# Kernel tuning notes

Hardware: AMD Instinct MI355X
Metric: run time of the kernel (lower is better)

The kernel has to match this reference:

```python
import jax, jax.numpy as jnp
import numpy as np

DIM = 1024      # input_size (C)
E = 8           # num_experts
TOPK = 2        # use_experts
MLP = 4 * DIM   # int(dim * mlp_ratio)
B, N = 4, 1024


def _gelu(v):
    # torch nn.GELU default = exact erf gelu
    return jax.nn.gelu(v, approximate=False)


def setup_inputs() -> dict:
    key = jax.random.key(0)
    ks = jax.random.split(key, 20)
    s = 0.02
    f32 = jnp.float32
    return {
        "x": jax.random.normal(ks[0], (B, N, DIM), f32),
        "prompt": jax.random.normal(ks[1], (B, N, DIM), f32),
        "t": jax.random.uniform(ks[2], (B, N, 1), f32) * 1000.0,
        # gating time_embedding MLP
        "te_w1": jax.random.normal(ks[3], (1, DIM), f32) * s,
        "te_b1": jnp.zeros((DIM,), f32),
        "te_w2": jax.random.normal(ks[4], (DIM, DIM), f32) * s,
        "te_b2": jnp.zeros((DIM,), f32),
        "gate_w": jax.random.normal(ks[5], (3 * DIM, E), f32) * s,
        # stacked per-expert params [E, ...]
        "ex_tw1": jax.random.normal(ks[6], (E, 1, DIM), f32) * s,
        "ex_tb1": jnp.zeros((E, DIM), f32),
        "ex_tw2": jax.random.normal(ks[7], (E, DIM, DIM), f32) * s,
        "ex_tb2": jnp.zeros((E, DIM), f32),
        "ex_mw1": jax.random.normal(ks[8], (E, 2 * DIM, MLP), f32) * s,
        "ex_mb1": jnp.zeros((E, MLP), f32),
        "ex_mw2": jax.random.normal(ks[9], (E, MLP, DIM), f32) * s,
        "ex_mb2": jnp.zeros((E, DIM), f32),
    }


def _forward(x, prompt, t, te_w1, te_b1, te_w2, te_b2, gate_w,
             ex_tw1, ex_tb1, ex_tw2, ex_tb2, ex_mw1, ex_mb1, ex_mw2, ex_mb2):
    Bb, Nn, C = x.shape
    xf = x.reshape(-1, C)            # [T, C]
    pf = prompt.reshape(-1, C)
    tf = t.reshape(-1, 1)            # [T, 1]
    T = xf.shape[0]

    # noisy_gate (eval: no noise)
    t_emb = _gelu(tf @ te_w1 + te_b1) @ te_w2 + te_b2          # [T, C]
    x_cat = jnp.concatenate([xf, pf, t_emb], axis=-1)          # [T, 3C]
    logits = x_cat @ gate_w                                    # [T, E]
    top_l, top_i = jax.lax.top_k(logits, TOPK)
    gates = jnp.zeros_like(logits).at[
        jnp.arange(T)[:, None], top_i
    ].set(jax.nn.softmax(top_l, axis=1))                       # [T, E]

    # per-expert diffusion MLP, dense over experts (gate==0 contributes 0,
    # identical math to dispatch/split/index_add combine)
    te = _gelu(jnp.einsum('to,eod->etd', tf, ex_tw1) + ex_tb1[:, None, :])
    te = jnp.einsum('etd,edf->etf', te, ex_tw2) + ex_tb2[:, None, :]   # [E,T,C]
    xc = jnp.concatenate([jnp.broadcast_to(xf, (E, T, C)), te], axis=-1)  # [E,T,2C]
    h = _gelu(jnp.einsum('etc,ech->eth', xc, ex_mw1) + ex_mb1[:, None, :])
    out_e = jnp.einsum('eth,ehd->etd', h, ex_mw2) + ex_mb2[:, None, :]    # [E,T,C]

    out_f = jnp.einsum('te,etd->td', gates, out_e)             # combine
    output = out_f.reshape(Bb, Nn, C)

    load = gates.sum(0)                                        # [E]
    eps = 1e-10
    bal = jnp.var(load, ddof=1) / (jnp.mean(load) ** 2 + eps)
    moe_loss = bal + bal  # weight_balance + load_balance (same argument)
    return output, moe_loss


def reference(x, prompt, t, te_w1, te_b1, te_w2, te_b2, gate_w,
              ex_tw1, ex_tb1, ex_tw2, ex_tb2, ex_mw1, ex_mb1, ex_mw2, ex_mb2):
    return _forward(x, prompt, t, te_w1, te_b1, te_w2, te_b2, gate_w,
                    ex_tw1, ex_tb1, ex_tw2, ex_tb2, ex_mw1, ex_mb1, ex_mw2, ex_mb2)
```

## Files before the change

### kernel.cpp

```cpp
#include <hip/hip_runtime.h>
#include <cmath>

#define TTOK 4096
#define CDIM 1024
#define NE 8
#define MLPD 4096
#define PCAP (2*TTOK + NE*128)

typedef __attribute__((ext_vector_type(8))) short short8;
typedef __attribute__((ext_vector_type(8))) unsigned short us8;
typedef __attribute__((ext_vector_type(4))) float float4v;

__device__ __forceinline__ float bf2f(unsigned short h){
  return __uint_as_float(((unsigned int)h) << 16);
}
__device__ __forceinline__ unsigned short f2bf(float f){
  unsigned int u = __float_as_uint(f);
  u += 0x7FFFu + ((u >> 16) & 1u);
  return (unsigned short)(u >> 16);
}
__device__ __forceinline__ float gelu_exact(float x){
  return 0.5f * x * (1.0f + erff(x * 0.70710678118654752f));
}
__device__ __forceinline__ void gld16(const void* g, void* l){
  __builtin_amdgcn_global_load_lds((const __attribute__((address_space(1))) void*)g,
                                   (__attribute__((address_space(3))) void*)l, 16, 0, 0);
}
__device__ __forceinline__ int frag_off(int m, int qf){
  return (m*4 + ((qf + (m >> 1)) & 3)) << 3;
}
__device__ __forceinline__ void xcd_swz(int& bx, int& by){
  int gx = gridDim.x, gy = gridDim.y;
  int orig = blockIdx.y * gx + blockIdx.x;
  int chunk = (gx * gy) >> 3;
  int wg = (orig & 7) * chunk + (orig >> 3);
  bx = wg / gy;
  by = wg % gy;
}

__global__ __launch_bounds__(256) void k_zero(float* out, int n, int* counts, float* loadsum){
  int i = blockIdx.x*256 + threadIdx.x;
  if (i < n) out[i] = 0.f;
  if (i < NE){ counts[i] = 0; loadsum[i] = 0.f; }
}

__global__ __launch_bounds__(256) void k_m2(const float* __restrict__ te_w2,
    const float* __restrict__ te_b2, const float* __restrict__ gate_w,
    float* __restrict__ M2, float* __restrict__ c2){
  int idx = blockIdx.x*256 + threadIdx.x;
  if (idx < CDIM*NE){
    int i = idx >> 3, e = idx & 7;
    float s = 0.f;
    for (int j = 0; j < CDIM; j++)
      s += te_w2[(size_t)i*CDIM + j] * gate_w[(size_t)(2*CDIM + j)*NE + e];
    M2[idx] = s;
  } else if (idx < CDIM*NE + NE){
    int e = idx - CDIM*NE;
    float s = 0.f;
    for (int j = 0; j < CDIM; j++)
      s += te_b2[j] * gate_w[(size_t)(2*CDIM + j)*NE + e];
    c2[e] = s;
  }
}

__global__ __launch_bounds__(256) void k_cvt_w(const float* __restrict__ W,
    unsigned short* __restrict__ Wt, int K, int N){
  __shared__ unsigned short tile[64*66];
  int kb = blockIdx.x*64, nb = blockIdx.y*64, e = blockIdx.z;
  const float* Wp = W + (size_t)e*K*N + (size_t)kb*N + nb;
  unsigned short* Wo = Wt + (size_t)e*K*N + (size_t)nb*K + kb;
  int tid = threadIdx.x;
  int kr = tid >> 4, nc = (tid & 15)*4;
  #pragma unroll
  for (int i = 0; i < 64; i += 16){
    float4 v = *reinterpret_cast<const float4*>(Wp + (size_t)(kr + i)*N + nc);
    unsigned short* d = &tile[(kr + i)*66 + nc];
    d[0] = f2bf(v.x); d[1] = f2bf(v.y); d[2] = f2bf(v.z); d[3] = f2bf(v.w);
  }
  __syncthreads();
  int nr = tid >> 2, kc = (tid & 3)*16;
  #pragma unroll
  for (int h = 0; h < 2; h++){
    us8 o;
    #pragma unroll
    for (int j = 0; j < 8; j++) o[j] = tile[(kc + h*8 + j)*66 + nr];
    *reinterpret_cast<us8*>(Wo + (size_t)nr*K + kc + h*8) = o;
  }
}

__global__ __launch_bounds__(256) void k_gate(const float* __restrict__ x,
    const float* __restrict__ p, const float* __restrict__ t,
    const float* __restrict__ te_w1, const float* __restrict__ te_b1,
    const float* __restrict__ gate_w, const float* __restrict__ M2,
    const float* __restrict__ c2,
    int* __restrict__ ti, float* __restrict__ tg,
    int* __restrict__ counts, float* __restrict__ loadsum,
    unsigned short* __restrict__ xb){
  int tok = blockIdx.x, tid = threadIdx.x;
  float tv = t[tok];
  float acc[NE];
  #pragma unroll
  for (int e = 0; e < NE; e++) acc[e] = 0.f;
  for (int j = tid; j < CDIM; j += 256){
    float xv = x[(size_t)tok*CDIM + j];
    float pv = p[(size_t)tok*CDIM + j];
    if (xb) xb[(size_t)tok*CDIM + j] = f2bf(xv);
    float vv = gelu_exact(tv*te_w1[j] + te_b1[j]);
    const float* g0 = gate_w + (size_t)j*NE;
    const float* g1 = gate_w + (size_t)(CDIM + j)*NE;
    const float* m2 = M2 + (size_t)j*NE;
    #pragma unroll
    for (int e = 0; e < NE; e++) acc[e] += xv*g0[e] + pv*g1[e] + vv*m2[e];
  }
  __shared__ float red[256][NE];
  #pragma unroll
  for (int e = 0; e < NE; e++) red[tid][e] = acc[e];
  __syncthreads();
  for (int s = 128; s > 0; s >>= 1){
    if (tid < s){
      #pragma unroll
      for (int e = 0; e < NE; e++) red[tid][e] += red[tid+s][e];
    }
    __syncthreads();
  }
  if (tid == 0){
    float lg[NE];
    #pragma unroll
    for (int e = 0; e < NE; e++) lg[e] = red[0][e] + c2[e];
    int i1 = 0; float l1 = lg[0];
    #pragma unroll
    for (int e = 1; e < NE; e++) if (lg[e] > l1){ l1 = lg[e]; i1 = e; }
    int i2 = -1; float l2 = -3.4e38f;
    #pragma unroll
    for (int e = 0; e < NE; e++) if (e != i1 && lg[e] > l2){ l2 = lg[e]; i2 = e; }
    float ex  = expf(l2 - l1);
    float g1v = 1.f/(1.f + ex);
    float g2v = ex/(1.f + ex);
    ti[tok*2]   = i1; ti[tok*2+1] = i2;
    tg[tok*2]   = g1v; tg[tok*2+1] = g2v;
    atomicAdd(&counts[i1], 1);  atomicAdd(&counts[i2], 1);
    atomicAdd(&loadsum[i1], g1v); atomicAdd(&loadsum[i2], g2v);
  }
}

__global__ __launch_bounds__(256) void k_scan(const int* __restrict__ counts,
    int* __restrict__ poff, int* __restrict__ fillpos,
    int* __restrict__ tok_id, float* __restrict__ pgate, int* __restrict__ pe, int padg){
  __shared__ int so[NE+1];
  __shared__ int sc[NE];
  if (threadIdx.x == 0){
    int o = 0;
    for (int e = 0; e < NE; e++){
      so[e] = o; poff[e] = o; fillpos[e] = o;
      sc[e] = counts[e];
      o += (sc[e] + padg - 1) & ~(padg - 1);
    }
    so[NE] = o; poff[NE] = o;
  }
  __syncthreads();
  for (int e = 0; e < NE; e++){
    int s = so[e] + sc[e], en = so[e+1];
    for (int i = s + (int)threadIdx.x; i < en; i += 256){
      tok_id[i] = 0; pgate[i] = 0.f; pe[i] = e;
    }
  }
}

__global__ __launch_bounds__(256) void k_fill(const int* __restrict__ ti,
    const float* __restrict__ tg, int* __restrict__ fillpos,
    int* __restrict__ tok_id, float* __restrict__ pgate, int* __restrict__ pe,
    int* __restrict__ posmap){
  int tok = blockIdx.x*256 + threadIdx.x;
  if (tok >= TTOK) return;
  #pragma unroll
  for (int k = 0; k < 2; k++){
    int e = ti[tok*2 + k];
    int pos = atomicAdd(&fillpos[e], 1);
    tok_id[pos] = tok;
    pgate[pos]  = tg[tok*2 + k];
    pe[pos]     = e;
    posmap[tok*2 + k] = pos;
  }
}

__global__ __launch_bounds__(256) void k_vgelu(const float* __restrict__ t,
    const float* __restrict__ tw1, const float* __restrict__ tb1,
    const int* __restrict__ tok_id, const int* __restrict__ pe,
    const int* __restrict__ poff, unsigned short* __restrict__ vbuf){
  int idx = blockIdx.x*256 + threadIdx.x;
  int r = idx >> 10, k = idx & (CDIM - 1);
  if (r >= poff[NE]) return;
  int e = pe[r];
  float tv = t[tok_id[r]];
  float u = tv * tw1[(size_t)e*CDIM + k] + tb1[(size_t)e*CDIM + k];
  vbuf[(size_t)r*CDIM + k] = f2bf(gelu_exact(u));
}


__global__ __launch_bounds__(256,2) void k_mfma_te(
    const unsigned short* __restrict__ vbuf,
    const unsigned short* __restrict__ Wt1, const float* __restrict__ tb2,
    const int* __restrict__ poff, const int* __restrict__ pe,
    unsigned short* __restrict__ tebuf){
  __shared__ unsigned short As[128*32];
  __shared__ unsigned short Bs[128*32];
  int bx, by; xcd_swz(bx, by);
  int r0 = by * 128;
  if (r0 >= poff[NE]) return;
  int e = pe[r0];
  int n0 = bx * 128;
  int tid = threadIdx.x, lane = tid & 63, w = tid >> 6;
  const unsigned short* Bp = Wt1 + (size_t)e*CDIM*CDIM;
  int mb = (w&1)*64, nb = (w>>1)*64;
  float4v acc[4][4];
  #pragma unroll
  for (int i=0;i<4;i++)
    #pragma unroll
    for (int j=0;j<4;j++) acc[i][j] = (float4v){0.f,0.f,0.f,0.f};
  int rowA = w*32 + (lane>>2);
  int ck = (((lane & 3) - ((lane >> 3) & 3)) & 3) * 8;
  int r15 = lane & 15, qf = lane >> 4;
  for (int k0 = 0; k0 < CDIM; k0 += 32){
    __syncthreads();
    unsigned short* lA = As + (w*32)*32;
    unsigned short* lB = Bs + (w*32)*32;
    gld16(vbuf + (size_t)(r0+rowA)*CDIM + k0 + ck, lA);
    gld16(vbuf + (size_t)(r0+rowA+16)*CDIM + k0 + ck, lA + 16*32);
    gld16(Bp + (size_t)(n0+rowA)*CDIM + k0 + ck, lB);
    gld16(Bp + (size_t)(n0+rowA+16)*CDIM + k0 + ck, lB + 16*32);
    __syncthreads();
    short8 a[4], b[4];
    #pragma unroll
    for (int mi=0;mi<4;mi++) a[mi] = *(const short8*)(As + frag_off(mb+mi*16+r15, qf));
    #pragma unroll
    for (int ni=0;ni<4;ni++) b[ni] = *(const short8*)(Bs + frag_off(nb+ni*16+r15, qf));
    #pragma unroll
    for (int mi=0;mi<4;mi++)
      #pragma unroll
      for (int ni=0;ni<4;ni++)
        acc[mi][ni] = __builtin_amdgcn_mfma_f32_16x16x32_bf16(a[mi], b[ni], acc[mi][ni], 0, 0, 0);
  }
  int col = lane & 15, rq = (lane>>4)*4;
  const float* bias = tb2 + (size_t)e*CDIM + n0;
  #pragma unroll
  for (int mi=0;mi<4;mi++)
    #pragma unroll
    for (int ni=0;ni<4;ni++){
      int n = nb + ni*16 + col;
      #pragma unroll
      for (int rg=0;rg<4;rg++){
        int r = r0 + mb + mi*16 + rq + rg;
        tebuf[(size_t)r*CDIM + n0 + n] = f2bf(acc[mi][ni][rg] + bias[n]);
      }
    }
}

__global__ __launch_bounds__(256,2) void k_mfma_h(
    const unsigned short* __restrict__ xb, const unsigned short* __restrict__ tebuf,
    const unsigned short* __restrict__ Wt2, const float* __restrict__ mb1,
    const int* __restrict__ poff, const int* __restrict__ pe,
    const int* __restrict__ tok_id, unsigned short* __restrict__ hbuf){
  __shared__ unsigned short As[128*32];
  __shared__ unsigned short Bs[128*32];
  __shared__ int toks[128];
  int bx, by; xcd_swz(bx, by);
  int r0 = by * 128;
  if (r0 >= poff[NE]) return;
  int e = pe[r0];
  int n0 = bx * 128;
  int tid = threadIdx.x, lane = tid & 63, w = tid >> 6;
  if (tid < 128) toks[tid] = tok_id[r0 + tid];
  const unsigned short* Bp = Wt2 + (size_t)e*(2*CDIM)*MLPD;
  int mb = (w&1)*64, nb = (w>>1)*64;
  float4v acc[4][4];
  #pragma unroll
  for (int i=0;i<4;i++)
    #pragma unroll
    for (int j=0;j<4;j++) acc[i][j] = (float4v){0.f,0.f,0.f,0.f};
  int rowA = w*32 + (lane>>2);
  int ck = (((lane & 3) - ((lane >> 3) & 3)) & 3) * 8;
  int r15 = lane & 15, qf = lane >> 4;
  __syncthreads();
  for (int k0 = 0; k0 < 2*CDIM; k0 += 32){
    __syncthreads();
    unsigned short* lA = As + (w*32)*32;
    unsigned short* lB = Bs + (w*32)*32;
    if (k0 < CDIM){
      int tok0 = toks[rowA], tok1 = toks[rowA+16];
      gld16(xb + (size_t)tok0*CDIM + k0 + ck, lA);
      gld16(xb + (size_t)tok1*CDIM + k0 + ck, lA + 16*32);
    } else {
      gld16(tebuf + (size_t)(r0+rowA)*CDIM + (k0-CDIM) + ck, lA);
      gld16(tebuf + (size_t)(r0+rowA+16)*CDIM + (k0-CDIM) + ck, lA + 16*32);
    }
    gld16(Bp + (size_t)(n0+rowA)*(2*CDIM) + k0 + ck, lB);
    gld16(Bp + (size_t)(n0+rowA+16)*(2*CDIM) + k0 + ck, lB + 16*32);
    __syncthreads();
    short8 a[4], b[4];
    #pragma unroll
    for (int mi=0;mi<4;mi++) a[mi] = *(const short8*)(As + frag_off(mb+mi*16+r15, qf));
    #pragma unroll
    for (int ni=0;ni<4;ni++) b[ni] = *(const short8*)(Bs + frag_off(nb+ni*16+r15, qf));
    #pragma unroll
    for (int mi=0;mi<4;mi++)
      #pragma unroll
      for (int ni=0;ni<4;ni++)
        acc[mi][ni] = __builtin_amdgcn_mfma_f32_16x16x32_bf16(a[mi], b[ni], acc[mi][ni], 0, 0, 0);
  }
  int col = lane & 15, rq = (lane>>4)*4;
  const float* bias = mb1 + (size_t)e*MLPD + n0;
  #pragma unroll
  for (int mi=0;mi<4;mi++)
    #pragma unroll
    for (int ni=0;ni<4;ni++){
      int n = nb + ni*16 + col;
      #pragma unroll
      for (int rg=0;rg<4;rg++){
        int r = r0 + mb + mi*16 + rq + rg;
        hbuf[(size_t)r*MLPD + n0 + n] = f2bf(gelu_exact(acc[mi][ni][rg] + bias[n]));
      }
    }
}

__global__ __launch_bounds__(256,2) void k_mfma_out(
    const unsigned short* __restrict__ hbuf,
    const unsigned short* __restrict__ Wt3, const float* __restrict__ mb2,
    const int* __restrict__ poff, const int* __restrict__ pe,
    float* __restrict__ obuf){
  __shared__ unsigned short As[128*32];
  __shared__ unsigned short Bs[128*32];
  int bx, by; xcd_swz(bx, by);
  int r0 = by * 128;
  if (r0 >= poff[NE]) return;
  int e = pe[r0];
  int n0 = bx * 128;
  int tid = threadIdx.x, lane = tid & 63, w = tid >> 6;
  const unsigned short* Bp = Wt3 + (size_t)e*MLPD*CDIM;
  int mb = (w&1)*64, nb = (w>>1)*64;
  float4v acc[4][4];
  #pragma unroll
  for (int i=0;i<4;i++)
    #pragma unroll
    for (int j=0;j<4;j++) acc[i][j] = (float4v){0.f,0.f,0.f,0.f};
  int rowA = w*32 + (lane>>2);
  int ck = (((lane & 3) - ((lane >> 3) & 3)) & 3) * 8;
  int r15 = lane & 15, qf = lane >> 4;
  for (int k0 = 0; k0 < MLPD; k0 += 32){
    __syncthreads();
    unsigned short* lA = As + (w*32)*32;
    unsigned short* lB = Bs + (w*32)*32;
    gld16(hbuf + (size_t)(r0+rowA)*MLPD + k0 + ck, lA);
    gld16(hbuf + (size_t)(r0+rowA+16)*MLPD + k0 + ck, lA + 16*32);
    gld16(Bp + (size_t)(n0+rowA)*MLPD + k0 + ck, lB);
    gld16(Bp + (size_t)(n0+rowA+16)*MLPD + k0 + ck, lB + 16*32);
    __syncthreads();
    short8 a[4], b[4];
    #pragma unroll
    for (int mi=0;mi<4;mi++) a[mi] = *(const short8*)(As + frag_off(mb+mi*16+r15, qf));
    #pragma unroll
    for (int ni=0;ni<4;ni++) b[ni] = *(const short8*)(Bs + frag_off(nb+ni*16+r15, qf));
    #pragma unroll
    for (int mi=0;mi<4;mi++)
      #pragma unroll
      for (int ni=0;ni<4;ni++)
        acc[mi][ni] = __builtin_amdgcn_mfma_f32_16x16x32_bf16(a[mi], b[ni], acc[mi][ni], 0, 0, 0);
  }
  int col = lane & 15, rq = (lane>>4)*4;
  const float* bias = mb2 + (size_t)e*CDIM + n0;
  #pragma unroll
  for (int mi=0;mi<4;mi++)
    #pragma unroll
    for (int ni=0;ni<4;ni++){
      int n = nb + ni*16 + col;
      #pragma unroll
      for (int rg=0;rg<4;rg++){
        int r = r0 + mb + mi*16 + rq + rg;
        obuf[(size_t)r*CDIM + n0 + n] = acc[mi][ni][rg] + bias[n];
      }
    }
}

__global__ __launch_bounds__(256) void k_combine(const float* __restrict__ obuf,
    const int* __restrict__ posmap, const float* __restrict__ tg,
    float* __restrict__ out){
  int idx = blockIdx.x*256 + threadIdx.x;
  int tok = idx >> 8, n4 = (idx & 255)*4;
  int p1 = posmap[tok*2], p2 = posmap[tok*2+1];
  float g1 = tg[tok*2], g2 = tg[tok*2+1];
  float4 a = *reinterpret_cast<const float4*>(obuf + (size_t)p1*CDIM + n4);
  float4 b = *reinterpret_cast<const float4*>(obuf + (size_t)p2*CDIM + n4);
  float4 o;
  o.x = g1*a.x + g2*b.x; o.y = g1*a.y + g2*b.y;
  o.z = g1*a.z + g2*b.z; o.w = g1*a.w + g2*b.w;
  *reinterpret_cast<float4*>(out + (size_t)tok*CDIM + n4) = o;
}

__global__ __launch_bounds__(256) void k_gemm_te_f(
    const unsigned short* __restrict__ vbuf,
    const float* __restrict__ tw2, const float* __restrict__ tb2,
    const int* __restrict__ poff, const int* __restrict__ pe,
    unsigned short* __restrict__ tebuf){
  int r0 = blockIdx.y * 64;
  if (r0 >= poff[NE]) return;
  int e = pe[r0];
  int n0 = blockIdx.x * 64;
  const float* Bp = tw2 + (size_t)e*CDIM*CDIM;
  __shared__ float As[16][68];
  __shared__ float Bs[16][68];
  int tid = threadIdx.x;
  int tx = tid & 15, ty = tid >> 4;
  int lm = tid >> 2, lk = (tid & 3)*4;
  int bk = tid >> 4, bn = (tid & 15)*4;
  float acc[4][4] = {{0.f}};
  for (int k0 = 0; k0 < CDIM; k0 += 16){
    ushort4 av = *reinterpret_cast<const ushort4*>(vbuf + (size_t)(r0+lm)*CDIM + k0 + lk);
    float4  bv = *reinterpret_cast<const float4*>(Bp + (size_t)(k0+bk)*CDIM + n0 + bn);
    __syncthreads();
    As[lk+0][lm] = bf2f(av.x); As[lk+1][lm] = bf2f(av.y);
    As[lk+2][lm] = bf2f(av.z); As[lk+3][lm] = bf2f(av.w);
    *reinterpret_cast<float4*>(&Bs[bk][bn]) = bv;
    __syncthreads();
    #pragma unroll
    for (int k = 0; k < 16; k++){
      float4 a = *reinterpret_cast<const float4*>(&As[k][ty*4]);
      float4 b = *reinterpret_cast<const float4*>(&Bs[k][tx*4]);
      float am[4] = {a.x,a.y,a.z,a.w}, bn4[4] = {b.x,b.y,b.z,b.w};
      #pragma unroll
      for (int i = 0; i < 4; i++)
        #pragma unroll
        for (int j = 0; j < 4; j++) acc[i][j] += am[i]*bn4[j];
    }
  }
  #pragma unroll
  for (int i = 0; i < 4; i++){
    int r = r0 + ty*4 + i;
    #pragma unroll
    for (int j = 0; j < 4; j++){
      int n = n0 + tx*4 + j;
      tebuf[(size_t)r*CDIM + n] = f2bf(acc[i][j] + tb2[(size_t)e*CDIM + n]);
    }
  }
}

__global__ __launch_bounds__(256) void k_gemm_h_f(
    const float* __restrict__ x, const unsigned short* __restrict__ tebuf,
    const float* __restrict__ mw1, const float* __restrict__ mb1,
    const int* __restrict__ poff, const int* __restrict__ pe,
    const int* __restrict__ tok_id, unsigned short* __restrict__ hbuf){
  int r0 = blockIdx.y * 64;
  if (r0 >= poff[NE]) return;
  int e = pe[r0];
  int n0 = blockIdx.x * 64;
  const float* Bp = mw1 + (size_t)e*(2*CDIM)*MLPD;
  __shared__ float As[16][68];
  __shared__ float Bs[16][68];
  __shared__ int toks[64];
  int tid = threadIdx.x;
  if (tid < 64) toks[tid] = tok_id[r0 + tid];
  int tx = tid & 15, ty = tid >> 4;
  int lm = tid >> 2, lk = (tid & 3)*4;
  int bk = tid >> 4, bn = (tid & 15)*4;
  float acc[4][4] = {{0.f}};
  __syncthreads();
  for (int k0 = 0; k0 < 2*CDIM; k0 += 16){
    float4 af;
    if (k0 < CDIM){
      af = *reinterpret_cast<const float4*>(x + (size_t)toks[lm]*CDIM + k0 + lk);
    } else {
      ushort4 av = *reinterpret_cast<const ushort4*>(tebuf + (size_t)(r0+lm)*CDIM + (k0 - CDIM) + lk);
      af.x = bf2f(av.x); af.y = bf2f(av.y); af.z = bf2f(av.z); af.w = bf2f(av.w);
    }
    float4 bv = *reinterpret_cast<const float4*>(Bp + (size_t)(k0+bk)*MLPD + n0 + bn);
    __syncthreads();
    As[lk+0][lm] = af.x; As[lk+1][lm] = af.y;
    As[lk+2][lm] = af.z; As[lk+3][lm] = af.w;
    *reinterpret_cast<float4*>(&Bs[bk][bn]) = bv;
    __syncthreads();
    #pragma unroll
    for (int k = 0; k < 16; k++){
      float4 a = *reinterpret_cast<const float4*>(&As[k][ty*4]);
      float4 b = *reinterpret_cast<const float4*>(&Bs[k][tx*4]);
      float am[4] = {a.x,a.y,a.z,a.w}, bn4[4] = {b.x,b.y,b.z,b.w};
      #pragma unroll
      for (int i = 0; i < 4; i++)
        #pragma unroll
        for (int j = 0; j < 4; j++) acc[i][j] += am[i]*bn4[j];
    }
  }
  #pragma unroll
  for (int i = 0; i < 4; i++){
    int r = r0 + ty*4 + i;
    #pragma unroll
    for (int j = 0; j < 4; j++){
      int n = n0 + tx*4 + j;
      hbuf[(size_t)r*MLPD + n] = f2bf(gelu_exact(acc[i][j] + mb1[(size_t)e*MLPD + n]));
    }
  }
}

__global__ __launch_bounds__(256) void k_gemm_out_f(
    const unsigned short* __restrict__ hbuf,
    const float* __restrict__ mw2, const float* __restrict__ mb2,
    const int* __restrict__ poff, const int* __restrict__ pe,
    const int* __restrict__ tok_id, const float* __restrict__ pgate,
    float* __restrict__ out){
  int r0 = blockIdx.y * 64;
  if (r0 >= poff[NE]) return;
  int e = pe[r0];
  int n0 = blockIdx.x * 64;
  const float* Bp = mw2 + (size_t)e*MLPD*CDIM;
  __shared__ float As[16][68];
  __shared__ float Bs[16][68];
  __shared__ int   toks[64];
  __shared__ float gts[64];
  int tid = threadIdx.x;
  if (tid < 64){ toks[tid] = tok_id[r0 + tid]; gts[tid] = pgate[r0 + tid]; }
  int tx = tid & 15, ty = tid >> 4;
  int lm = tid >> 2, lk = (tid & 3)*4;
  int bk = tid >> 4, bn = (tid & 15)*4;
  float acc[4][4] = {{0.f}};
  __syncthreads();
  for (int k0 = 0; k0 < MLPD; k0 += 16){
    ushort4 av = *reinterpret_cast<const ushort4*>(hbuf + (size_t)(r0+lm)*MLPD + k0 + lk);
    float4  bv = *reinterpret_cast<const float4*>(Bp + (size_t)(k0+bk)*CDIM + n0 + bn);
    __syncthreads();
    As[lk+0][lm] = bf2f(av.x); As[lk+1][lm] = bf2f(av.y);
    As[lk+2][lm] = bf2f(av.z); As[lk+3][lm] = bf2f(av.w);
    *reinterpret_cast<float4*>(&Bs[bk][bn]) = bv;
    __syncthreads();
    #pragma unroll
    for (int k = 0; k < 16; k++){
      float4 a = *reinterpret_cast<const float4*>(&As[k][ty*4]);
      float4 b = *reinterpret_cast<const float4*>(&Bs[k][tx*4]);
      float am[4] = {a.x,a.y,a.z,a.w}, bn4[4] = {b.x,b.y,b.z,b.w};
      #pragma unroll
      for (int i = 0; i < 4; i++)
        #pragma unroll
        for (int j = 0; j < 4; j++) acc[i][j] += am[i]*bn4[j];
    }
  }
  #pragma unroll
  for (int i = 0; i < 4; i++){
    int rl = ty*4 + i;
    int tok = toks[rl];
    float g = gts[rl];
    #pragma unroll
    for (int j = 0; j < 4; j++){
      int n = n0 + tx*4 + j;
      float val = acc[i][j] + mb2[(size_t)e*CDIM + n];
      atomicAdd(&out[(size_t)tok*CDIM + n], g*val);
    }
  }
}

__global__ void k_loss(const float* __restrict__ loadsum, float* __restrict__ outp){
  if (threadIdx.x == 0 && blockIdx.x == 0){
    float m = 0.f;
    for (int e = 0; e < NE; e++) m += loadsum[e];
    m *= (1.f/NE);
    float v = 0.f;
    for (int e = 0; e < NE; e++){ float d = loadsum[e] - m; v += d*d; }
    v *= (1.f/(NE-1));
    float bal = v / (m*m + 1e-10f);
    outp[0] = 2.f * bal;
  }
}

extern "C" void kernel_launch(void* const* d_in, const int* in_sizes, int n_in,
                              void* d_out, int out_size, void* d_ws, size_t ws_size,
                              hipStream_t stream){
  const float* x      = (const float*)d_in[0];
  const float* p      = (const float*)d_in[1];
  const float* t      = (const float*)d_in[2];
  const float* te_w1  = (const float*)d_in[3];
  const float* te_b1  = (const float*)d_in[4];
  const float* te_w2  = (const float*)d_in[5];
  const float* te_b2  = (const float*)d_in[6];
  const float* gate_w = (const float*)d_in[7];
  const float* ex_tw1 = (const float*)d_in[8];
  const float* ex_tb1 = (const float*)d_in[9];
  const float* ex_tw2 = (const float*)d_in[10];
  const float* ex_tb2 = (const float*)d_in[11];
  const float* ex_mw1 = (const float*)d_in[12];
  const float* ex_mb1 = (const float*)d_in[13];
  const float* ex_mw2 = (const float*)d_in[14];
  const float* ex_mb2 = (const float*)d_in[15];
  float* out = (float*)d_out;

  char* ws = (char*)d_ws;
  size_t off = 0;
  auto take = [&](size_t b){ size_t r = off; off = (off + b + 255) & ~(size_t)255; return r; };
  int*   counts  = (int*)  (ws + take(NE*sizeof(int)));
  int*   fillpos = (int*)  (ws + take(NE*sizeof(int)));
  int*   poff    = (int*)  (ws + take((NE+1)*sizeof(int)));
  float* loadsum = (float*)(ws + take(NE*sizeof(float)));
  float* M2      = (float*)(ws + take((size_t)CDIM*NE*sizeof(float)));
  float* c2      = (float*)(ws + take(NE*sizeof(float)));
  int*   ti      = (int*)  (ws + take((size_t)TTOK*2*sizeof(int)));
  float* tg      = (float*)(ws + take((size_t)TTOK*2*sizeof(float)));
  int*   posmap  = (int*)  (ws + take((size_t)TTOK*2*sizeof(int)));
  int*   tok_id  = (int*)  (ws + take((size_t)PCAP*sizeof(int)));
  float* pgate   = (float*)(ws + take((size_t)PCAP*sizeof(float)));
  int*   pe      = (int*)  (ws + take((size_t)PCAP*sizeof(int)));

  size_t need_mfma = off
      + ((size_t)TTOK*CDIM*2 + 256)
      + ((size_t)PCAP*MLPD*2 + 256)
      + ((size_t)PCAP*CDIM*2 + 256)
      + ((size_t)NE*2*CDIM*MLPD*2 + 256);
  bool use_mfma = ws_size >= need_mfma;
  int padg = use_mfma ? 128 : 64;

  int nOut = use_mfma ? 0 : (TTOK*CDIM + 1);
  int zBlocks = use_mfma ? 1 : (nOut + 255)/256;
  k_zero<<<dim3(zBlocks), dim3(256), 0, stream>>>(out, nOut, counts, loadsum);
  k_m2<<<dim3((CDIM*NE + NE + 255)/256), dim3(256), 0, stream>>>(te_w2, te_b2, gate_w, M2, c2);

  if (use_mfma){
    unsigned short* xb    = (unsigned short*)(ws + take((size_t)TTOK*CDIM*2));
    char*           hreg  = ws + take((size_t)PCAP*MLPD*2);
    unsigned short* vbuf  = (unsigned short*)hreg;
    unsigned short* Wt1   = (unsigned short*)(hreg + (size_t)PCAP*CDIM*2);
    unsigned short* hbuf  = (unsigned short*)hreg;
    unsigned short* tebuf = (unsigned short*)(ws + take((size_t)PCAP*CDIM*2));
    unsigned short* Wt2   = (unsigned short*)(ws + take((size_t)NE*2*CDIM*MLPD*2));
    unsigned short* Wt3   = Wt2;
    float*          obuf  = (float*)(Wt2 + (size_t)NE*MLPD*CDIM);

    k_gate<<<dim3(TTOK), dim3(256), 0, stream>>>(x, p, t, te_w1, te_b1, gate_w, M2, c2,
                                                 ti, tg, counts, loadsum, xb);
    k_scan<<<dim3(1), dim3(256), 0, stream>>>(counts, poff, fillpos, tok_id, pgate, pe, padg);
    k_fill<<<dim3((TTOK + 255)/256), dim3(256), 0, stream>>>(ti, tg, fillpos, tok_id, pgate, pe, posmap);
    k_cvt_w<<<dim3(CDIM/64, CDIM/64, NE), dim3(256), 0, stream>>>(ex_tw2, Wt1, CDIM, CDIM);
    k_cvt_w<<<dim3(2*CDIM/64, MLPD/64, NE), dim3(256), 0, stream>>>(ex_mw1, Wt2, 2*CDIM, MLPD);
    k_vgelu<<<dim3((PCAP*CDIM)/256), dim3(256), 0, stream>>>(t, ex_tw1, ex_tb1, tok_id, pe, poff, vbuf);
    k_mfma_te<<<dim3(CDIM/128, PCAP/128), dim3(256), 0, stream>>>(vbuf, Wt1, ex_tb2, poff, pe, tebuf);
    k_mfma_h<<<dim3(MLPD/128, PCAP/128), dim3(256), 0, stream>>>(xb, tebuf, Wt2, ex_mb1,
                                                                 poff, pe, tok_id, hbuf);
    k_cvt_w<<<dim3(MLPD/64, CDIM/64, NE), dim3(256), 0, stream>>>(ex_mw2, Wt3, MLPD, CDIM);
    k_mfma_out<<<dim3(CDIM/128, PCAP/128), dim3(256), 0, stream>>>(hbuf, Wt3, ex_mb2,
                                                                   poff, pe, obuf);
    k_combine<<<dim3((TTOK*CDIM/4)/256), dim3(256), 0, stream>>>(obuf, posmap, tg, out);
  } else {
    unsigned short* vbuf  = (unsigned short*)(ws + take((size_t)PCAP*MLPD*2));
    unsigned short* hbuf  = vbuf;
    unsigned short* tebuf = (unsigned short*)(ws + take((size_t)PCAP*CDIM*2));
    k_gate<<<dim3(TTOK), dim3(256), 0, stream>>>(x, p, t, te_w1, te_b1, gate_w, M2, c2,
                                                 ti, tg, counts, loadsum, (unsigned short*)nullptr);
    k_scan<<<dim3(1), dim3(256), 0, stream>>>(counts, poff, fillpos, tok_id, pgate, pe, padg);
    k_fill<<<dim3((TTOK + 255)/256), dim3(256), 0, stream>>>(ti, tg, fillpos, tok_id, pgate, pe, posmap);
    k_vgelu<<<dim3((PCAP*CDIM)/256), dim3(256), 0, stream>>>(t, ex_tw1, ex_tb1, tok_id, pe, poff, vbuf);
    k_gemm_te_f<<<dim3(CDIM/64, PCAP/64), dim3(256), 0, stream>>>(vbuf, ex_tw2, ex_tb2, poff, pe, tebuf);
    k_gemm_h_f<<<dim3(MLPD/64, PCAP/64), dim3(256), 0, stream>>>(x, tebuf, ex_mw1, ex_mb1,
                                                                 poff, pe, tok_id, hbuf);
    k_gemm_out_f<<<dim3(CDIM/64, PCAP/64), dim3(256), 0, stream>>>(hbuf, ex_mw2, ex_mb2,
                                                                   poff, pe, tok_id, pgate, out);
  }
  k_loss<<<dim3(1), dim3(64), 0, stream>>>(loadsum, out + (size_t)TTOK*CDIM);
}
```

Baseline: 1.187 ms.

## Double-buffer LDS tiles in expert MFMA GEMM kernels to overlap loads

The three expert GEMM kernels (time-embedding, hidden and output projections) now use two LDS buffers per operand. The next K-tile is issued into the spare buffer while MFMAs consume the current one, with one barrier per iteration instead of two. This aims to hide global-to-LDS load latency behind compute. LDS use per block doubles to 32 KB, which could limit occupancy alongside the launch bound of two blocks.

```diff
diff --git a/kernel.cpp b/kernel.cpp
--- a/kernel.cpp
+++ b/kernel.cpp
@@ -202,8 +202,8 @@
     const unsigned short* __restrict__ Wt1, const float* __restrict__ tb2,
     const int* __restrict__ poff, const int* __restrict__ pe,
     unsigned short* __restrict__ tebuf){
-  __shared__ unsigned short As[128*32];
-  __shared__ unsigned short Bs[128*32];
+  __shared__ unsigned short As[2][128*32];
+  __shared__ unsigned short Bs[2][128*32];
   int bx, by; xcd_swz(bx, by);
   int r0 = by * 128;
   if (r0 >= poff[NE]) return;
@@ -220,25 +220,37 @@
   int rowA = w*32 + (lane>>2);
   int ck = (((lane & 3) - ((lane >> 3) & 3)) & 3) * 8;
   int r15 = lane & 15, qf = lane >> 4;
-  for (int k0 = 0; k0 < CDIM; k0 += 32){
-    __syncthreads();
-    unsigned short* lA = As + (w*32)*32;
-    unsigned short* lB = Bs + (w*32)*32;
-    gld16(vbuf + (size_t)(r0+rowA)*CDIM + k0 + ck, lA);
-    gld16(vbuf + (size_t)(r0+rowA+16)*CDIM + k0 + ck, lA + 16*32);
-    gld16(Bp + (size_t)(n0+rowA)*CDIM + k0 + ck, lB);
-    gld16(Bp + (size_t)(n0+rowA+16)*CDIM + k0 + ck, lB + 16*32);
-    __syncthreads();
+  int wo = (w*32)*32;
+  const unsigned short* gA0 = vbuf + (size_t)(r0+rowA)*CDIM + ck;
+  const unsigned short* gA1 = vbuf + (size_t)(r0+rowA+16)*CDIM + ck;
+  const unsigned short* gB0 = Bp + (size_t)(n0+rowA)*CDIM + ck;
+  const unsigned short* gB1 = Bp + (size_t)(n0+rowA+16)*CDIM + ck;
+  gld16(gA0, &As[0][wo]); gld16(gA1, &As[0][wo + 16*32]);
+  gld16(gB0, &Bs[0][wo]); gld16(gB1, &Bs[0][wo + 16*32]);
+  __syncthreads();
+  const int NK = CDIM/32;
+  for (int i = 0; i < NK; i++){
+    int cur = i & 1;
+    if (i + 1 < NK){
+      int kk = (i + 1) * 32;
+      unsigned short* lA = &As[cur^1][wo];
+      unsigned short* lB = &Bs[cur^1][wo];
+      gld16(gA0 + kk, lA); gld16(gA1 + kk, lA + 16*32);
+      gld16(gB0 + kk, lB); gld16(gB1 + kk, lB + 16*32);
+    }
+    const unsigned short* cA = &As[cur][0];
+    const unsigned short* cB = &Bs[cur][0];
     short8 a[4], b[4];
     #pragma unroll
-    for (int mi=0;mi<4;mi++) a[mi] = *(const short8*)(As + frag_off(mb+mi*16+r15, qf));
-    #pragma unroll
-    for (int ni=0;ni<4;ni++) b[ni] = *(const short8*)(Bs + frag_off(nb+ni*16+r15, qf));
+    for (int mi=0;mi<4;mi++) a[mi] = *(const short8*)(cA + frag_off(mb+mi*16+r15, qf));
+    #pragma unroll
+    for (int ni=0;ni<4;ni++) b[ni] = *(const short8*)(cB + frag_off(nb+ni*16+r15, qf));
     #pragma unroll
     for (int mi=0;mi<4;mi++)
       #pragma unroll
       for (int ni=0;ni<4;ni++)
         acc[mi][ni] = __builtin_amdgcn_mfma_f32_16x16x32_bf16(a[mi], b[ni], acc[mi][ni], 0, 0, 0);
+    __syncthreads();
   }
   int col = lane & 15, rq = (lane>>4)*4;
   const float* bias = tb2 + (size_t)e*CDIM + n0;
@@ -260,8 +272,8 @@
     const unsigned short* __restrict__ Wt2, const float* __restrict__ mb1,
     const int* __restrict__ poff, const int* __restrict__ pe,
     const int* __restrict__ tok_id, unsigned short* __restrict__ hbuf){
-  __shared__ unsigned short As[128*32];
-  __shared__ unsigned short Bs[128*32];
+  __shared__ unsigned short As[2][128*32];
+  __shared__ unsigned short Bs[2][128*32];
   __shared__ int toks[128];
   int bx, by; xcd_swz(bx, by);
   int r0 = by * 128;
@@ -280,32 +292,45 @@
   int rowA = w*32 + (lane>>2);
   int ck = (((lane & 3) - ((lane >> 3) & 3)) & 3) * 8;
   int r15 = lane & 15, qf = lane >> 4;
-  __syncthreads();
-  for (int k0 = 0; k0 < 2*CDIM; k0 += 32){
-    __syncthreads();
-    unsigned short* lA = As + (w*32)*32;
-    unsigned short* lB = Bs + (w*32)*32;
-    if (k0 < CDIM){
-      int tok0 = toks[rowA], tok1 = toks[rowA+16];
-      gld16(xb + (size_t)tok0*CDIM + k0 + ck, lA);
-      gld16(xb + (size_t)tok1*CDIM + k0 + ck, lA + 16*32);
-    } else {
-      gld16(tebuf + (size_t)(r0+rowA)*CDIM + (k0-CDIM) + ck, lA);
-      gld16(tebuf + (size_t)(r0+rowA+16)*CDIM + (k0-CDIM) + ck, lA + 16*32);
-    }
-    gld16(Bp + (size_t)(n0+rowA)*(2*CDIM) + k0 + ck, lB);
-    gld16(Bp + (size_t)(n0+rowA+16)*(2*CDIM) + k0 + ck, lB + 16*32);
-    __syncthreads();
+  int wo = (w*32)*32;
+  __syncthreads();
+  int tok0 = toks[rowA], tok1 = toks[rowA + 16];
+  const unsigned short* gX0 = xb + (size_t)tok0*CDIM + ck;
+  const unsigned short* gX1 = xb + (size_t)tok1*CDIM + ck;
+  const unsigned short* gT0 = tebuf + (size_t)(r0+rowA)*CDIM + ck;
+  const unsigned short* gT1 = tebuf + (size_t)(r0+rowA+16)*CDIM + ck;
+  const unsigned short* gB0 = Bp + (size_t)(n0+rowA)*(2*CDIM) + ck;
+  const unsigned short* gB1 = Bp + (size_t)(n0+rowA+16)*(2*CDIM) + ck;
+  gld16(gX0, &As[0][wo]); gld16(gX1, &As[0][wo + 16*32]);
+  gld16(gB0, &Bs[0][wo]); gld16(gB1, &Bs[0][wo + 16*32]);
+  __syncthreads();
+  const int NK = (2*CDIM)/32;
+  for (int i = 0; i < NK; i++){
+    int cur = i & 1;
+    if (i + 1 < NK){
+      int kk = (i + 1) * 32;
+      unsigned short* lA = &As[cur^1][wo];
+      unsigned short* lB = &Bs[cur^1][wo];
+      if (kk < CDIM){
+        gld16(gX0 + kk, lA); gld16(gX1 + kk, lA + 16*32);
+      } else {
+        gld16(gT0 + (kk - CDIM), lA); gld16(gT1 + (kk - CDIM), lA + 16*32);
+      }
+      gld16(gB0 + kk, lB); gld16(gB1 + kk, lB + 16*32);
+    }
+    const unsigned short* cA = &As[cur][0];
+    const unsigned short* cB = &Bs[cur][0];
     short8 a[4], b[4];
     #pragma unroll
-    for (int mi=0;mi<4;mi++) a[mi] = *(const short8*)(As + frag_off(mb+mi*16+r15, qf));
-    #pragma unroll
-    for (int ni=0;ni<4;ni++) b[ni] = *(const short8*)(Bs + frag_off(nb+ni*16+r15, qf));
+    for (int mi=0;mi<4;mi++) a[mi] = *(const short8*)(cA + frag_off(mb+mi*16+r15, qf));
+    #pragma unroll
+    for (int ni=0;ni<4;ni++) b[ni] = *(const short8*)(cB + frag_off(nb+ni*16+r15, qf));
     #pragma unroll
     for (int mi=0;mi<4;mi++)
       #pragma unroll
       for (int ni=0;ni<4;ni++)
         acc[mi][ni] = __builtin_amdgcn_mfma_f32_16x16x32_bf16(a[mi], b[ni], acc[mi][ni], 0, 0, 0);
+    __syncthreads();
   }
   int col = lane & 15, rq = (lane>>4)*4;
   const float* bias = mb1 + (size_t)e*MLPD + n0;
@@ -327,8 +352,8 @@
     const unsigned short* __restrict__ Wt3, const float* __restrict__ mb2,
     const int* __restrict__ poff, const int* __restrict__ pe,
     float* __restrict__ obuf){
-  __shared__ unsigned short As[128*32];
-  __shared__ unsigned short Bs[128*32];
+  __shared__ unsigned short As[2][128*32];
+  __shared__ unsigned short Bs[2][128*32];
   int bx, by; xcd_swz(bx, by);
   int r0 = by * 128;
   if (r0 >= poff[NE]) return;
@@ -345,25 +370,37 @@
   int rowA = w*32 + (lane>>2);
   int ck = (((lane & 3) - ((lane >> 3) & 3)) & 3) * 8;
   int r15 = lane & 15, qf = lane >> 4;
-  for (int k0 = 0; k0 < MLPD; k0 += 32){
-    __syncthreads();
-    unsigned short* lA = As + (w*32)*32;
-    unsigned short* lB = Bs + (w*32)*32;
-    gld16(hbuf + (size_t)(r0+rowA)*MLPD + k0 + ck, lA);
-    gld16(hbuf + (size_t)(r0+rowA+16)*MLPD + k0 + ck, lA + 16*32);
-    gld16(Bp + (size_t)(n0+rowA)*MLPD + k0 + ck, lB);
-    gld16(Bp + (size_t)(n0+rowA+16)*MLPD + k0 + ck, lB + 16*32);
-    __syncthreads();
+  int wo = (w*32)*32;
+  const unsigned short* gA0 = hbuf + (size_t)(r0+rowA)*MLPD + ck;
+  const unsigned short* gA1 = hbuf + (size_t)(r0+rowA+16)*MLPD + ck;
+  const unsigned short* gB0 = Bp + (size_t)(n0+rowA)*MLPD + ck;
+  const unsigned short* gB1 = Bp + (size_t)(n0+rowA+16)*MLPD + ck;
+  gld16(gA0, &As[0][wo]); gld16(gA1, &As[0][wo + 16*32]);
+  gld16(gB0, &Bs[0][wo]); gld16(gB1, &Bs[0][wo + 16*32]);
+  __syncthreads();
+  const int NK = MLPD/32;
+  for (int i = 0; i < NK; i++){
+    int cur = i & 1;
+    if (i + 1 < NK){
+      int kk = (i + 1) * 32;
+      unsigned short* lA = &As[cur^1][wo];
+      unsigned short* lB = &Bs[cur^1][wo];
+      gld16(gA0 + kk, lA); gld16(gA1 + kk, lA + 16*32);
+      gld16(gB0 + kk, lB); gld16(gB1 + kk, lB + 16*32);
+    }
+    const unsigned short* cA = &As[cur][0];
+    const unsigned short* cB = &Bs[cur][0];
     short8 a[4], b[4];
     #pragma unroll
-    for (int mi=0;mi<4;mi++) a[mi] = *(const short8*)(As + frag_off(mb+mi*16+r15, qf));
-    #pragma unroll
-    for (int ni=0;ni<4;ni++) b[ni] = *(const short8*)(Bs + frag_off(nb+ni*16+r15, qf));
+    for (int mi=0;mi<4;mi++) a[mi] = *(const short8*)(cA + frag_off(mb+mi*16+r15, qf));
+    #pragma unroll
+    for (int ni=0;ni<4;ni++) b[ni] = *(const short8*)(cB + frag_off(nb+ni*16+r15, qf));
     #pragma unroll
     for (int mi=0;mi<4;mi++)
       #pragma unroll
       for (int ni=0;ni<4;ni++)
         acc[mi][ni] = __builtin_amdgcn_mfma_f32_16x16x32_bf16(a[mi], b[ni], acc[mi][ni], 0, 0, 0);
+    __syncthreads();
   }
   int col = lane & 15, rq = (lane>>4)*4;
   const float* bias = mb2 + (size_t)e*CDIM + n0;
```

Result: no change. 1.193 ms (+0.5%).

## Double K-tile depth to 64 with XOR-swizzled LDS, fold zero/loss kernels

Applied to the files above, without the earlier changes.

The three expert MFMA GEMMs now stage 64-wide K slices per iteration instead of 32. They use an XOR swizzle for LDS layout and fragment reads, and hoist the global row pointers out of the loop. This halves the number of barrier pairs per GEMM and aims to cut LDS bank conflicts, at the cost of twice the shared memory per block. Separately, the zero kernel and the loss kernel are folded into k_m2 and k_combine on the MFMA path, removing two small launches.

```diff
diff --git a/kernel.cpp b/kernel.cpp
--- a/kernel.cpp
+++ b/kernel.cpp
@@ -26,8 +26,8 @@
   __builtin_amdgcn_global_load_lds((const __attribute__((address_space(1))) void*)g,
                                    (__attribute__((address_space(3))) void*)l, 16, 0, 0);
 }
-__device__ __forceinline__ int frag_off(int m, int qf){
-  return (m*4 + ((qf + (m >> 1)) & 3)) << 3;
+__device__ __forceinline__ int foff64(int m, int q){
+  return (m << 6) + ((q ^ (m & 7)) << 3);
 }
 __device__ __forceinline__ void xcd_swz(int& bx, int& by){
   int gx = gridDim.x, gy = gridDim.y;
@@ -46,8 +46,10 @@
 
 __global__ __launch_bounds__(256) void k_m2(const float* __restrict__ te_w2,
     const float* __restrict__ te_b2, const float* __restrict__ gate_w,
-    float* __restrict__ M2, float* __restrict__ c2){
+    float* __restrict__ M2, float* __restrict__ c2,
+    int* __restrict__ counts, float* __restrict__ loadsum){
   int idx = blockIdx.x*256 + threadIdx.x;
+  if (idx < NE){ counts[idx] = 0; loadsum[idx] = 0.f; }
   if (idx < CDIM*NE){
     int i = idx >> 3, e = idx & 7;
     float s = 0.f;
@@ -202,8 +204,8 @@
     const unsigned short* __restrict__ Wt1, const float* __restrict__ tb2,
     const int* __restrict__ poff, const int* __restrict__ pe,
     unsigned short* __restrict__ tebuf){
-  __shared__ unsigned short As[128*32];
-  __shared__ unsigned short Bs[128*32];
+  __shared__ unsigned short As[128*64];
+  __shared__ unsigned short Bs[128*64];
   int bx, by; xcd_swz(bx, by);
   int r0 = by * 128;
   if (r0 >= poff[NE]) return;
@@ -217,28 +219,34 @@
   for (int i=0;i<4;i++)
     #pragma unroll
     for (int j=0;j<4;j++) acc[i][j] = (float4v){0.f,0.f,0.f,0.f};
-  int rowA = w*32 + (lane>>2);
-  int ck = (((lane & 3) - ((lane >> 3) & 3)) & 3) * 8;
+  int rowA = w*32 + (lane>>3);
+  int ck = (((lane & 7) ^ ((lane >> 3) & 7)) << 3);
   int r15 = lane & 15, qf = lane >> 4;
-  for (int k0 = 0; k0 < CDIM; k0 += 32){
-    __syncthreads();
-    unsigned short* lA = As + (w*32)*32;
-    unsigned short* lB = Bs + (w*32)*32;
-    gld16(vbuf + (size_t)(r0+rowA)*CDIM + k0 + ck, lA);
-    gld16(vbuf + (size_t)(r0+rowA+16)*CDIM + k0 + ck, lA + 16*32);
-    gld16(Bp + (size_t)(n0+rowA)*CDIM + k0 + ck, lB);
-    gld16(Bp + (size_t)(n0+rowA+16)*CDIM + k0 + ck, lB + 16*32);
-    __syncthreads();
-    short8 a[4], b[4];
-    #pragma unroll
-    for (int mi=0;mi<4;mi++) a[mi] = *(const short8*)(As + frag_off(mb+mi*16+r15, qf));
-    #pragma unroll
-    for (int ni=0;ni<4;ni++) b[ni] = *(const short8*)(Bs + frag_off(nb+ni*16+r15, qf));
-    #pragma unroll
-    for (int mi=0;mi<4;mi++)
-      #pragma unroll
-      for (int ni=0;ni<4;ni++)
-        acc[mi][ni] = __builtin_amdgcn_mfma_f32_16x16x32_bf16(a[mi], b[ni], acc[mi][ni], 0, 0, 0);
+  unsigned short* lA = As + (w*32)*64;
+  unsigned short* lB = Bs + (w*32)*64;
+  const unsigned short* gA = vbuf + (size_t)(r0+rowA)*CDIM + ck;
+  const unsigned short* gB = Bp + (size_t)(n0+rowA)*CDIM + ck;
+  for (int k0 = 0; k0 < CDIM; k0 += 64){
+    __syncthreads();
+    #pragma unroll
+    for (int d = 0; d < 4; d++){
+      gld16(gA + (size_t)(d*8)*CDIM + k0, lA + d*8*64);
+      gld16(gB + (size_t)(d*8)*CDIM + k0, lB + d*8*64);
+    }
+    __syncthreads();
+    #pragma unroll
+    for (int half = 0; half < 2; half++){
+      short8 a[4], b[4];
+      #pragma unroll
+      for (int mi=0;mi<4;mi++) a[mi] = *(const short8*)(As + foff64(mb+mi*16+r15, half*4 + qf));
+      #pragma unroll
+      for (int ni=0;ni<4;ni++) b[ni] = *(const short8*)(Bs + foff64(nb+ni*16+r15, half*4 + qf));
+      #pragma unroll
+      for (int mi=0;mi<4;mi++)
+        #pragma unroll
+        for (int ni=0;ni<4;ni++)
+          acc[mi][ni] = __builtin_amdgcn_mfma_f32_16x16x32_bf16(a[mi], b[ni], acc[mi][ni], 0, 0, 0);
+    }
   }
   int col = lane & 15, rq = (lane>>4)*4;
   const float* bias = tb2 + (size_t)e*CDIM + n0;
@@ -260,8 +268,8 @@
     const unsigned short* __restrict__ Wt2, const float* __restrict__ mb1,
     const int* __restrict__ poff, const int* __restrict__ pe,
     const int* __restrict__ tok_id, unsigned short* __restrict__ hbuf){
-  __shared__ unsigned short As[128*32];
-  __shared__ unsigned short Bs[128*32];
+  __shared__ unsigned short As[128*64];
+  __shared__ unsigned short Bs[128*64];
   __shared__ int toks[128];
   int bx, by; xcd_swz(bx, by);
   int r0 = by * 128;
@@ -277,35 +285,46 @@
   for (int i=0;i<4;i++)
     #pragma unroll
     for (int j=0;j<4;j++) acc[i][j] = (float4v){0.f,0.f,0.f,0.f};
-  int rowA = w*32 + (lane>>2);
-  int ck = (((lane & 3) - ((lane >> 3) & 3)) & 3) * 8;
+  int rowA = w*32 + (lane>>3);
+  int ck = (((lane & 7) ^ ((lane >> 3) & 7)) << 3);
   int r15 = lane & 15, qf = lane >> 4;
+  unsigned short* lA = As + (w*32)*64;
+  unsigned short* lB = Bs + (w*32)*64;
   __syncthreads();
-  for (int k0 = 0; k0 < 2*CDIM; k0 += 32){
-    __syncthreads();
-    unsigned short* lA = As + (w*32)*32;
-    unsigned short* lB = Bs + (w*32)*32;
+  const unsigned short* gX[4];
+  const unsigned short* gT[4];
+  #pragma unroll
+  for (int d = 0; d < 4; d++){
+    gX[d] = xb + (size_t)toks[rowA + d*8]*CDIM + ck;
+    gT[d] = tebuf + (size_t)(r0 + rowA + d*8)*CDIM + ck;
+  }
+  const unsigned short* gB = Bp + (size_t)(n0+rowA)*(2*CDIM) + ck;
+  for (int k0 = 0; k0 < 2*CDIM; k0 += 64){
+    __syncthreads();
     if (k0 < CDIM){
-      int tok0 = toks[rowA], tok1 = toks[rowA+16];
-      gld16(xb + (size_t)tok0*CDIM + k0 + ck, lA);
-      gld16(xb + (size_t)tok1*CDIM + k0 + ck, lA + 16*32);
+      #pragma unroll
+      for (int d = 0; d < 4; d++) gld16(gX[d] + k0, lA + d*8*64);
     } else {
-      gld16(tebuf + (size_t)(r0+rowA)*CDIM + (k0-CDIM) + ck, lA);
-      gld16(tebuf + (size_t)(r0+rowA+16)*CDIM + (k0-CDIM) + ck, lA + 16*32);
-    }
-    gld16(Bp + (size_t)(n0+rowA)*(2*CDIM) + k0 + ck, lB);
-    gld16(Bp + (size_t)(n0+rowA+16)*(2*CDIM) + k0 + ck, lB + 16*32);
-    __syncthreads();
-    short8 a[4], b[4];
-    #pragma unroll
-    for (int mi=0;mi<4;mi++) a[mi] = *(const short8*)(As + frag_off(mb+mi*16+r15, qf));
-    #pragma unroll
-    for (int ni=0;ni<4;ni++) b[ni] = *(const short8*)(Bs + frag_off(nb+ni*16+r15, qf));
-    #pragma unroll
-    for (int mi=0;mi<4;mi++)
-      #pragma unroll
-      for (int ni=0;ni<4;ni++)
-        acc[mi][ni] = __builtin_amdgcn_mfma_f32_16x16x32_bf16(a[mi], b[ni], acc[mi][ni], 0, 0, 0);
+      #pragma unroll
+      for (int d = 0; d < 4; d++) gld16(gT[d] + (k0 - CDIM), lA + d*8*64);
+    }
+    #pragma unroll
+    for (int d = 0; d < 4; d++)
+      gld16(gB + (size_t)(d*8)*(2*CDIM) + k0, lB + d*8*64);
+    __syncthreads();
+    #pragma unroll
+    for (int half = 0; half < 2; half++){
+      short8 a[4], b[4];
+      #pragma unroll
+      for (int mi=0;mi<4;mi++) a[mi] = *(const short8*)(As + foff64(mb+mi*16+r15, half*4 + qf));
+      #pragma unroll
+      for (int ni=0;ni<4;ni++) b[ni] = *(const short8*)(Bs + foff64(nb+ni*16+r15, half*4 + qf));
+      #pragma unroll
+      for (int mi=0;mi<4;mi++)
+        #pragma unroll
+        for (int ni=0;ni<4;ni++)
+          acc[mi][ni] = __builtin_amdgcn_mfma_f32_16x16x32_bf16(a[mi], b[ni], acc[mi][ni], 0, 0, 0);
+    }
   }
   int col = lane & 15, rq = (lane>>4)*4;
   const float* bias = mb1 + (size_t)e*MLPD + n0;
@@ -327,8 +346,8 @@
     const unsigned short* __restrict__ Wt3, const float* __restrict__ mb2,
     const int* __restrict__ poff, const int* __restrict__ pe,
     float* __restrict__ obuf){
-  __shared__ unsigned short As[128*32];
-  __shared__ unsigned short Bs[128*32];
+  __shared__ unsigned short As[128*64];
+  __shared__ unsigned short Bs[128*64];
   int bx, by; xcd_swz(bx, by);
   int r0 = by * 128;
   if (r0 >= poff[NE]) return;
@@ -342,28 +361,34 @@
   for (int i=0;i<4;i++)
     #pragma unroll
     for (int j=0;j<4;j++) acc[i][j] = (float4v){0.f,0.f,0.f,0.f};
-  int rowA = w*32 + (lane>>2);
-  int ck = (((lane & 3) - ((lane >> 3) & 3)) & 3) * 8;
+  int rowA = w*32 + (lane>>3);
+  int ck = (((lane & 7) ^ ((lane >> 3) & 7)) << 3);
   int r15 = lane & 15, qf = lane >> 4;
-  for (int k0 = 0; k0 < MLPD; k0 += 32){
-    __syncthreads();
-    unsigned short* lA = As + (w*32)*32;
-    unsigned short* lB = Bs + (w*32)*32;
-    gld16(hbuf + (size_t)(r0+rowA)*MLPD + k0 + ck, lA);
-    gld16(hbuf + (size_t)(r0+rowA+16)*MLPD + k0 + ck, lA + 16*32);
-    gld16(Bp + (size_t)(n0+rowA)*MLPD + k0 + ck, lB);
-    gld16(Bp + (size_t)(n0+rowA+16)*MLPD + k0 + ck, lB + 16*32);
-    __syncthreads();
-    short8 a[4], b[4];
-    #pragma unroll
-    for (int mi=0;mi<4;mi++) a[mi] = *(const short8*)(As + frag_off(mb+mi*16+r15, qf));
-    #pragma unroll
-    for (int ni=0;ni<4;ni++) b[ni] = *(const short8*)(Bs + frag_off(nb+ni*16+r15, qf));
-    #pragma unroll
-    for (int mi=0;mi<4;mi++)
-      #pragma unroll
-      for (int ni=0;ni<4;ni++)
-        acc[mi][ni] = __builtin_amdgcn_mfma_f32_16x16x32_bf16(a[mi], b[ni], acc[mi][ni], 0, 0, 0);
+  unsigned short* lA = As + (w*32)*64;
+  unsigned short* lB = Bs + (w*32)*64;
+  const unsigned short* gA = hbuf + (size_t)(r0+rowA)*MLPD + ck;
+  const unsigned short* gB = Bp + (size_t)(n0+rowA)*MLPD + ck;
+  for (int k0 = 0; k0 < MLPD; k0 += 64){
+    __syncthreads();
+    #pragma unroll
+    for (int d = 0; d < 4; d++){
+      gld16(gA + (size_t)(d*8)*MLPD + k0, lA + d*8*64);
+      gld16(gB + (size_t)(d*8)*MLPD + k0, lB + d*8*64);
+    }
+    __syncthreads();
+    #pragma unroll
+    for (int half = 0; half < 2; half++){
+      short8 a[4], b[4];
+      #pragma unroll
+      for (int mi=0;mi<4;mi++) a[mi] = *(const short8*)(As + foff64(mb+mi*16+r15, half*4 + qf));
+      #pragma unroll
+      for (int ni=0;ni<4;ni++) b[ni] = *(const short8*)(Bs + foff64(nb+ni*16+r15, half*4 + qf));
+      #pragma unroll
+      for (int mi=0;mi<4;mi++)
+        #pragma unroll
+        for (int ni=0;ni<4;ni++)
+          acc[mi][ni] = __builtin_amdgcn_mfma_f32_16x16x32_bf16(a[mi], b[ni], acc[mi][ni], 0, 0, 0);
+    }
   }
   int col = lane & 15, rq = (lane>>4)*4;
   const float* bias = mb2 + (size_t)e*CDIM + n0;
@@ -382,8 +407,17 @@
 
 __global__ __launch_bounds__(256) void k_combine(const float* __restrict__ obuf,
     const int* __restrict__ posmap, const float* __restrict__ tg,
-    float* __restrict__ out){
+    const float* __restrict__ loadsum, float* __restrict__ out){
   int idx = blockIdx.x*256 + threadIdx.x;
+  if (idx == 0){
+    float m = 0.f;
+    for (int e = 0; e < NE; e++) m += loadsum[e];
+    m *= (1.f/NE);
+    float v = 0.f;
+    for (int e = 0; e < NE; e++){ float d = loadsum[e] - m; v += d*d; }
+    v *= (1.f/(NE-1));
+    out[(size_t)TTOK*CDIM] = 2.f * (v / (m*m + 1e-10f));
+  }
   int tok = idx >> 8, n4 = (idx & 255)*4;
   int p1 = posmap[tok*2], p2 = posmap[tok*2+1];
   float g1 = tg[tok*2], g2 = tg[tok*2+1];
@@ -611,10 +645,12 @@
   bool use_mfma = ws_size >= need_mfma;
   int padg = use_mfma ? 128 : 64;
 
-  int nOut = use_mfma ? 0 : (TTOK*CDIM + 1);
-  int zBlocks = use_mfma ? 1 : (nOut + 255)/256;
-  k_zero<<<dim3(zBlocks), dim3(256), 0, stream>>>(out, nOut, counts, loadsum);
-  k_m2<<<dim3((CDIM*NE + NE + 255)/256), dim3(256), 0, stream>>>(te_w2, te_b2, gate_w, M2, c2);
+  if (!use_mfma){
+    int nOut = TTOK*CDIM + 1;
+    k_zero<<<dim3((nOut + 255)/256), dim3(256), 0, stream>>>(out, nOut, counts, loadsum);
+  }
+  k_m2<<<dim3((CDIM*NE + NE + 255)/256), dim3(256), 0, stream>>>(te_w2, te_b2, gate_w,
+                                                                 M2, c2, counts, loadsum);
 
   if (use_mfma){
     unsigned short* xb    = (unsigned short*)(ws + take((size_t)TTOK*CDIM*2));
@@ -640,7 +676,7 @@
     k_cvt_w<<<dim3(MLPD/64, CDIM/64, NE), dim3(256), 0, stream>>>(ex_mw2, Wt3, MLPD, CDIM);
     k_mfma_out<<<dim3(CDIM/128, PCAP/128), dim3(256), 0, stream>>>(hbuf, Wt3, ex_mb2,
                                                                    poff, pe, obuf);
-    k_combine<<<dim3((TTOK*CDIM/4)/256), dim3(256), 0, stream>>>(obuf, posmap, tg, out);
+    k_combine<<<dim3((TTOK*CDIM/4)/256), dim3(256), 0, stream>>>(obuf, posmap, tg, loadsum, out);
   } else {
     unsigned short* vbuf  = (unsigned short*)(ws + take((size_t)PCAP*MLPD*2));
     unsigned short* hbuf  = vbuf;
@@ -655,6 +691,6 @@
                                                                  poff, pe, tok_id, hbuf);
     k_gemm_out_f<<<dim3(CDIM/64, PCAP/64), dim3(256), 0, stream>>>(hbuf, ex_mw2, ex_mb2,
                                                                    poff, pe, tok_id, pgate, out);
-  }
-  k_loss<<<dim3(1), dim3(64), 0, stream>>>(loadsum, out + (size_t)TTOK*CDIM);
-}
+    k_loss<<<dim3(1), dim3(64), 0, stream>>>(loadsum, out + (size_t)TTOK*CDIM);
+  }
+}
```

Result: faster. 1.126 ms (-5.2%).
